# Optimization experiments

Measured on AMD Instinct MI355X. Metric: run time of the kernel, lower is better.

## Reference

```python
import jax, jax.numpy as jnp
import numpy as np

B, L, E = 512, 50, 512
VOCAB = 32000
EPS = 1e-5


def setup_inputs() -> dict:
    key = jax.random.key(0)
    ks = jax.random.split(key, 16)
    inp = {
        'src_tokens': jax.random.randint(ks[0], (B, L), 0, VOCAB, dtype=jnp.int32),
        'trg_tokens': jax.random.randint(ks[1], (B, L), 0, VOCAB, dtype=jnp.int32),
        'pad_idx': 1,
        'emb_src': jax.random.normal(ks[2], (VOCAB, E), jnp.float32) * 0.02,
        'emb_trg': jax.random.normal(ks[3], (VOCAB, E), jnp.float32) * 0.02,
        'W1': jax.random.normal(ks[4], (20, E), jnp.float32) / np.sqrt(E),  # Conv1d(1,20,k=E) kernel squeezed
        'b1': jax.random.normal(ks[5], (20,), jnp.float32) * 0.01,
        'g1': jnp.ones((20,), jnp.float32),
        'beta1': jnp.zeros((20,), jnp.float32),
        'W2': jax.random.normal(ks[6], (40, 20, 3, 3), jnp.float32) / np.sqrt(20 * 9),
        'b2': jax.random.normal(ks[7], (40,), jnp.float32) * 0.01,
        'g2': jnp.ones((40,), jnp.float32),
        'beta2': jnp.zeros((40,), jnp.float32),
        'Wfc1': jax.random.normal(ks[8], (20, 40 * 11 * 11), jnp.float32) / np.sqrt(40 * 11 * 11),
        'bfc1': jnp.zeros((20,), jnp.float32),
        'Wfc2': jax.random.normal(ks[9], (1, 20), jnp.float32) / np.sqrt(20),
        'bfc2': jnp.zeros((1,), jnp.float32),
    }
    return inp


def _maxpool2(x):  # [B,C,H,W] -> 2x2/2 valid max pool
    return jax.lax.reduce_window(x, -jnp.inf, jax.lax.max, (1, 1, 2, 2), (1, 1, 2, 2), 'VALID')


def reference(src_tokens, trg_tokens, pad_idx, emb_src, emb_trg, W1, b1, g1, beta1,
              W2, b2, g2, beta2, Wfc1, bfc1, Wfc2, bfc2):
    src_e = emb_src[src_tokens]  # [B,L,E]
    trg_e = emb_trg[trg_tokens]  # [B,L,E]

    def conv1_bn_relu(x):
        # per-sample Conv1d(1,20,k=E): collapses E -> scalar per position/channel
        f = jnp.einsum('ble,ce->blc', x, W1) + b1  # [B,L,20]
        # per-sample BatchNorm1d in training mode: stats over the L positions of each sample
        mu = jnp.mean(f, axis=1, keepdims=True)
        var = jnp.var(f, axis=1, keepdims=True)  # biased, as torch uses for normalization
        f = (f - mu) * jax.lax.rsqrt(var + EPS) * g1 + beta1
        return jax.nn.relu(f)

    s = conv1_bn_relu(src_e)  # [B,L,20]
    t = conv1_bn_relu(trg_e)  # [B,L,20]

    # broadcast outer-sum: out[b,i,j,c] = s[b,j,c] + t[b,i,c]
    out = s[:, None, :, :] + t[:, :, None, :]          # [B,L,L,20]
    out = jnp.transpose(out, (0, 3, 1, 2))             # [B,20,L,L]
    out = _maxpool2(out)                                # [B,20,25,25]

    out = jax.lax.conv_general_dilated(out, W2, (1, 1), 'VALID') + b2[None, :, None, None]  # [B,40,23,23]
    # BatchNorm2d training mode: stats over (batch, H, W)
    mu = jnp.mean(out, axis=(0, 2, 3), keepdims=True)
    var = jnp.var(out, axis=(0, 2, 3), keepdims=True)
    out = (out - mu) * jax.lax.rsqrt(var + EPS) * g2[None, :, None, None] + beta2[None, :, None, None]
    out = jax.nn.relu(out)
    out = _maxpool2(out)                                # [B,40,11,11]

    out = out.reshape(out.shape[0], -1)                 # [B,4840]
    out = out @ Wfc1.T + bfc1
    out = out @ Wfc2.T + bfc2
    return jax.nn.sigmoid(out)                          # [B,1]
```

## Files before the change

kernel.cpp:

```cpp
#include <hip/hip_runtime.h>
#include <hip/hip_bf16.h>

#define EPS 1e-5f

__device__ __forceinline__ float bf2f(unsigned short u) {
  union { unsigned int i; float f; } x; x.i = ((unsigned int)u) << 16; return x.f;
}
__device__ __forceinline__ float loadp(const void* p, int i, bool f32) {
  return f32 ? ((const float*)p)[i] : bf2f(((const unsigned short*)p)[i]);
}
__device__ __forceinline__ bool detect_f32(const void* g1) {
  return ((const unsigned int*)g1)[0] == 0x3F800000u;
}

__global__ __launch_bounds__(256) void k0_prep(
    const void* __restrict__ W1, const void* __restrict__ W2,
    const void* __restrict__ Wfc1,
    const void* __restrict__ g1, const void* __restrict__ beta1,
    const void* __restrict__ g2, const void* __restrict__ beta2,
    const void* __restrict__ bfc1, const void* __restrict__ Wfc2,
    const void* __restrict__ bfc2,
    float* __restrict__ W1T, float* __restrict__ WT, float* __restrict__ WS,
    float* __restrict__ Wfc1T, float* __restrict__ prm)
{
  const bool f32 = detect_f32(g1);
  int g = blockIdx.x * 256 + threadIdx.x;
  const int NT = 64 * 256;
  for (int i = g; i < 512 * 20; i += NT) {
    int e = i / 20, c = i - e * 20;
    W1T[i] = loadp(W1, c * 512 + e, f32);
  }
  for (int i = g; i < 40 * 3 * 20; i += NT) {
    int o = i / 60, r = i - o * 60;
    int k = r / 20, c = r - k * 20;
    float st = 0.f, ss = 0.f;
    for (int q = 0; q < 3; ++q) {
      st += loadp(W2, ((o * 20 + c) * 3 + k) * 3 + q, f32);
      ss += loadp(W2, ((o * 20 + c) * 3 + q) * 3 + k, f32);
    }
    WT[(o * 3 + k) * 20 + c] = st;
    WS[(o * 3 + k) * 20 + c] = ss;
  }
  for (int i = g; i < 4840 * 20; i += NT) {
    int kk = i / 4840, idx = i - kk * 4840;
    Wfc1T[idx * 20 + kk] = loadp(Wfc1, i, f32);
  }
  if (g < 20)        prm[g] = loadp(g1,    g,       f32);
  else if (g < 40)   prm[g] = loadp(beta1, g - 20,  f32);
  else if (g < 80)   prm[g] = loadp(g2,    g - 40,  f32);
  else if (g < 120)  prm[g] = loadp(beta2, g - 80,  f32);
  else if (g < 140)  prm[g] = loadp(bfc1,  g - 120, f32);
  else if (g < 160)  prm[g] = loadp(Wfc2,  g - 140, f32);
  else if (g == 160) prm[g] = loadp(bfc2,  0,       f32);
}

__global__ __launch_bounds__(512, 8) void k12_fused(
    const int* __restrict__ src_tok, const int* __restrict__ trg_tok,
    const void* __restrict__ emb_src, const void* __restrict__ emb_trg,
    const void* __restrict__ g1flag,
    const float* __restrict__ W1T,
    const float* __restrict__ WT, const float* __restrict__ WS,
    const float* __restrict__ prm,
    float* __restrict__ C1, float* __restrict__ R, float* __restrict__ S2)
{
  __shared__ float partA[8 * 50 * 21];
  __shared__ float fl[1000];
  __shared__ float sc[20], sh[20];
  float* wl    = partA;
  float* pmax  = partA + 2400;
  float* convl = partA + 2900;

  const bool f32 = detect_f32(g1flag);
  int bb = blockIdx.x;
  int side = bb >> 9, b = bb & 511;
  int t = threadIdx.x;
  int lane = t & 63;
  int ch = __builtin_amdgcn_readfirstlane(t >> 6);

  float acc[20];
#pragma unroll
  for (int c = 0; c < 20; ++c) acc[c] = 0.f;
  if (lane < 50) {
    int tok = side ? trg_tok[b * 50 + lane] : src_tok[b * 50 + lane];
    const void* emb = side ? emb_trg : emb_src;
    if (f32) {
      const float4* rowp = (const float4*)((const float*)emb + (size_t)tok * 512 + ch * 64);
      for (int half = 0; half < 2; ++half) {
        float4 u[8];
#pragma unroll
        for (int q = 0; q < 8; ++q) u[q] = rowp[half * 8 + q];
#pragma unroll
        for (int q = 0; q < 8; ++q) {
          float v[4] = { u[q].x, u[q].y, u[q].z, u[q].w };
          const float* w = W1T + (ch * 64 + half * 32 + q * 4) * 20;
#pragma unroll
          for (int j = 0; j < 4; ++j)
#pragma unroll
            for (int c = 0; c < 20; ++c) acc[c] = fmaf(v[j], w[j * 20 + c], acc[c]);
        }
      }
    } else {
      const uint4* rowp = (const uint4*)((const unsigned short*)emb + (size_t)tok * 512 + ch * 64);
      uint4 u[8];
#pragma unroll
      for (int q = 0; q < 8; ++q) u[q] = rowp[q];
#pragma unroll
      for (int q = 0; q < 8; ++q) {
        const unsigned int* qu = (const unsigned int*)&u[q];
        float v[8];
#pragma unroll
        for (int j = 0; j < 4; ++j) {
          union { unsigned int i; float f; } lo, hi;
          lo.i = qu[j] << 16; hi.i = qu[j] & 0xffff0000u;
          v[2 * j] = lo.f; v[2 * j + 1] = hi.f;
        }
        const float* w = W1T + (ch * 64 + q * 8) * 20;
#pragma unroll
        for (int j = 0; j < 8; ++j)
#pragma unroll
          for (int c = 0; c < 20; ++c) acc[c] = fmaf(v[j], w[j * 20 + c], acc[c]);
      }
    }
    float* pp = &partA[(ch * 50 + lane) * 21];
#pragma unroll
    for (int c = 0; c < 20; ++c) pp[c] = acc[c];
  }
  __syncthreads();
  for (int i = t; i < 1000; i += 512) {
    int l = i / 20, c = i - l * 20;
    float s = 0.f;
#pragma unroll
    for (int c2 = 0; c2 < 8; ++c2) s += partA[(c2 * 50 + l) * 21 + c];
    fl[i] = s;
  }
  __syncthreads();
  {
    const float* wsrc = side ? WT : WS;
    for (int i = t; i < 2400; i += 512) wl[i] = wsrc[i];
  }
  if (t < 20) {
    float s = 0.f, s2 = 0.f;
#pragma unroll
    for (int l = 0; l < 50; ++l) { float v = fl[l * 20 + t]; s += v; s2 += v * v; }
    float mu = s * (1.0f / 50.0f);
    float var = s2 * (1.0f / 50.0f) - mu * mu;
    float k = prm[t] * rsqrtf(var + EPS);
    sc[t] = k; sh[t] = prm[20 + t] - k * mu;
  }
  __syncthreads();
  for (int i = t; i < 500; i += 512) {
    int p = i / 20, c = i - p * 20;
    float k = sc[c], s0 = sh[c];
    float v0 = fmaxf(k * fl[(2 * p) * 20 + c] + s0, 0.f);
    float v1 = fmaxf(k * fl[(2 * p + 1) * 20 + c] + s0, 0.f);
    pmax[i] = fmaxf(v0, v1);
  }
  __syncthreads();
  for (int i = t; i < 920; i += 512) {
    int o = i / 23, y = i - o * 23;
    float a = 0.f;
#pragma unroll
    for (int ky = 0; ky < 3; ++ky) {
      const float* wr = &wl[(o * 3 + ky) * 20];
      const float* pr = &pmax[(y + ky) * 20];
#pragma unroll
      for (int c = 0; c < 20; ++c) a = fmaf(wr[c], pr[c], a);
    }
    C1[((size_t)o * 1024 + bb) * 23 + y] = a;
    convl[o * 24 + y] = a;
  }
  __syncthreads();
  if (t < 40) {
    float s = 0.f, s2 = 0.f;
#pragma unroll
    for (int y = 0; y < 23; ++y) { float v = convl[t * 24 + y]; s += v; s2 += v * v; }
    R[t * 1024 + bb] = s;
    S2[t * 1024 + bb] = s2;
  }
}

__global__ __launch_bounds__(256) void k3_bn2(
    const float* __restrict__ R, const float* __restrict__ S2,
    const float* __restrict__ prm,
    float* __restrict__ bn2)
{
  int o = blockIdx.x, t = threadIdx.x;
  float s1a = 0, s2a = 0, s1b = 0, s2b = 0, sab = 0;
  for (int b = t; b < 512; b += 256) {
    float ra = R[o * 1024 + 512 + b], rb = R[o * 1024 + b];
    s1a += ra; s1b += rb; sab += ra * rb;
    s2a += S2[o * 1024 + 512 + b];
    s2b += S2[o * 1024 + b];
  }
  __shared__ float Rd[5][256];
  Rd[0][t] = s1a; Rd[1][t] = s2a; Rd[2][t] = s1b; Rd[3][t] = s2b; Rd[4][t] = sab;
  __syncthreads();
  for (int s = 128; s > 0; s >>= 1) {
    if (t < s) {
#pragma unroll
      for (int q = 0; q < 5; ++q) Rd[q][t] += Rd[q][t + s];
    }
    __syncthreads();
  }
  if (t == 0) {
    const float invN = 1.0f / (512.0f * 23.0f);
    float muA = Rd[0][0] * invN, muB = Rd[2][0] * invN;
    float ea2 = Rd[1][0] * invN - muA * muA;
    float eb2 = Rd[3][0] * invN - muB * muB;
    float cross = 2.0f * (Rd[4][0] * (1.0f / (529.0f * 512.0f)) - muA * muB);
    float var = ea2 + eb2 + cross;
    float k = prm[40 + o] * rsqrtf(var + EPS);
    bn2[o] = k;
    bn2[40 + o] = prm[80 + o] - k * (muA + muB);
  }
}

__global__ __launch_bounds__(512) void k4_fc(
    const float* __restrict__ C1,
    const float* __restrict__ bn2,
    const float* __restrict__ Wfc1T,
    const float* __restrict__ prm,
    const void* __restrict__ g1flag,
    void* __restrict__ outv)
{
  const bool f32 = detect_f32(g1flag);
  int b = blockIdx.x, t = threadIdx.x;
  int lane = t & 63, wv = t >> 6;
  __shared__ float mA[440], mB[440];
  __shared__ float k2s[40], c2s[40];
  __shared__ float wred[8][20];
  __shared__ float o1[20];
  if (t < 40) k2s[t] = bn2[t];
  else if (t < 80) c2s[t - 40] = bn2[t];
  __syncthreads();
  for (int i = t; i < 440; i += 512) {
    int o = i / 11, y = i - o * 11;
    const float* pa = C1 + ((size_t)o * 1024 + 512 + b) * 23;
    const float* pb = C1 + ((size_t)o * 1024 + b) * 23;
    float a0 = pa[2 * y], a1 = pa[2 * y + 1];
    float b0 = pb[2 * y], b1 = pb[2 * y + 1];
    if (k2s[o] >= 0.f) { mA[i] = fmaxf(a0, a1); mB[i] = fmaxf(b0, b1); }
    else               { mA[i] = fminf(a0, a1); mB[i] = fminf(b0, b1); }
  }
  __syncthreads();
  float acc[20];
#pragma unroll
  for (int c = 0; c < 20; ++c) acc[c] = 0.f;
  for (int idx = t; idx < 4840; idx += 512) {
    int o = idx / 121, r = idx - o * 121;
    int y = r / 11, x = r - y * 11;
    float p = fmaxf(k2s[o] * (mA[o * 11 + y] + mB[o * 11 + x]) + c2s[o], 0.f);
    const float* w = Wfc1T + idx * 20;
#pragma unroll
    for (int c = 0; c < 20; ++c) acc[c] = fmaf(p, w[c], acc[c]);
  }
#pragma unroll
  for (int c = 0; c < 20; ++c) {
    float v = acc[c];
    v += __shfl_xor(v, 32); v += __shfl_xor(v, 16); v += __shfl_xor(v, 8);
    v += __shfl_xor(v, 4);  v += __shfl_xor(v, 2);  v += __shfl_xor(v, 1);
    acc[c] = v;
  }
  if (lane == 0) {
#pragma unroll
    for (int c = 0; c < 20; ++c) wred[wv][c] = acc[c];
  }
  __syncthreads();
  if (t < 20) {
    float s = 0.f;
#pragma unroll
    for (int q = 0; q < 8; ++q) s += wred[q][t];
    o1[t] = s + prm[120 + t];
  }
  __syncthreads();
  if (t == 0) {
    float z = prm[160];
#pragma unroll
    for (int c = 0; c < 20; ++c) z = fmaf(prm[140 + c], o1[c], z);
    float sg = 1.0f / (1.0f + expf(-z));
    if (f32) ((float*)outv)[b] = sg;
    else     ((__hip_bfloat16*)outv)[b] = __float2bfloat16(sg);
  }
}

extern "C" void kernel_launch(void* const* d_in, const int* in_sizes, int n_in,
                              void* d_out, int out_size, void* d_ws, size_t ws_size,
                              hipStream_t stream) {
  const int* src_tok = (const int*)d_in[0];
  const int* trg_tok = (const int*)d_in[1];
  const void* emb_src = d_in[3];
  const void* emb_trg = d_in[4];
  const void* W1    = d_in[5];
  const void* g1    = d_in[7];
  const void* beta1 = d_in[8];
  const void* W2    = d_in[9];
  const void* g2    = d_in[11];
  const void* beta2 = d_in[12];
  const void* Wfc1  = d_in[13];
  const void* bfc1  = d_in[14];
  const void* Wfc2  = d_in[15];
  const void* bfc2  = d_in[16];

  char* ws = (char*)d_ws;
  float* W1T   = (float*)(ws + 0);
  float* WT    = (float*)(ws + 40960);
  float* WS    = (float*)(ws + 50560);
  float* Wfc1T = (float*)(ws + 60160);
  float* prm   = (float*)(ws + 447360);
  float* bn2   = (float*)(ws + 448384);
  float* R     = (float*)(ws + 448896);
  float* S2    = (float*)(ws + 612736);
  float* C1    = (float*)(ws + 776576);

  k0_prep<<<64, 256, 0, stream>>>(W1, W2, Wfc1, g1, beta1, g2, beta2, bfc1, Wfc2,
                                  bfc2, W1T, WT, WS, Wfc1T, prm);
  k12_fused<<<1024, 512, 0, stream>>>(src_tok, trg_tok, emb_src, emb_trg, g1,
                                      W1T, WT, WS, prm, C1, R, S2);
  k3_bn2<<<40, 256, 0, stream>>>(R, S2, prm, bn2);
  k4_fc<<<512, 512, 0, stream>>>(C1, bn2, Wfc1T, prm, g1, d_out);
}
```

Before: 202.9 us.

## Halve k12 block size, compact LDS into one buffer, make C1/R/S2 sample-major

The fused embedding/conv kernel now runs 256 threads per block, with 4 waves each covering 128 embedding elements instead of 8 waves covering 64. Its shared arrays are merged into a single 4200-float buffer, cutting LDS per block so more blocks can be resident. C1, R and S2 are now stored sample-major, giving contiguous writes per block, and the k3/k4 readers are updated to match. Sched barriers keep the embedding loads grouped ahead of the FMAs. In exchange, each wave does more serial FMA work with fewer waves in flight per block.

```diff
diff --git a/kernel.cpp b/kernel.cpp
--- a/kernel.cpp
+++ b/kernel.cpp
@@ -54,7 +54,7 @@
   else if (g == 160) prm[g] = loadp(bfc2,  0,       f32);
 }
 
-__global__ __launch_bounds__(512, 8) void k12_fused(
+__global__ __launch_bounds__(256, 6) void k12_fused(
     const int* __restrict__ src_tok, const int* __restrict__ trg_tok,
     const void* __restrict__ emb_src, const void* __restrict__ emb_trg,
     const void* __restrict__ g1flag,
@@ -63,12 +63,7 @@
     const float* __restrict__ prm,
     float* __restrict__ C1, float* __restrict__ R, float* __restrict__ S2)
 {
-  __shared__ float partA[8 * 50 * 21];
-  __shared__ float fl[1000];
-  __shared__ float sc[20], sh[20];
-  float* wl    = partA;
-  float* pmax  = partA + 2400;
-  float* convl = partA + 2900;
+  __shared__ float lds[4200];
 
   const bool f32 = detect_f32(g1flag);
   int bb = blockIdx.x;
@@ -84,15 +79,16 @@
     int tok = side ? trg_tok[b * 50 + lane] : src_tok[b * 50 + lane];
     const void* emb = side ? emb_trg : emb_src;
     if (f32) {
-      const float4* rowp = (const float4*)((const float*)emb + (size_t)tok * 512 + ch * 64);
-      for (int half = 0; half < 2; ++half) {
+      const float4* rowp = (const float4*)((const float*)emb + (size_t)tok * 512 + ch * 128);
+      for (int grp = 0; grp < 4; ++grp) {
         float4 u[8];
 #pragma unroll
-        for (int q = 0; q < 8; ++q) u[q] = rowp[half * 8 + q];
+        for (int q = 0; q < 8; ++q) u[q] = rowp[grp * 8 + q];
+        __builtin_amdgcn_sched_barrier(0);
 #pragma unroll
         for (int q = 0; q < 8; ++q) {
           float v[4] = { u[q].x, u[q].y, u[q].z, u[q].w };
-          const float* w = W1T + (ch * 64 + half * 32 + q * 4) * 20;
+          const float* w = W1T + (ch * 128 + grp * 32 + q * 4) * 20;
 #pragma unroll
           for (int j = 0; j < 4; ++j)
 #pragma unroll
@@ -100,82 +96,85 @@
         }
       }
     } else {
-      const uint4* rowp = (const uint4*)((const unsigned short*)emb + (size_t)tok * 512 + ch * 64);
-      uint4 u[8];
-#pragma unroll
-      for (int q = 0; q < 8; ++q) u[q] = rowp[q];
-#pragma unroll
-      for (int q = 0; q < 8; ++q) {
-        const unsigned int* qu = (const unsigned int*)&u[q];
-        float v[8];
-#pragma unroll
-        for (int j = 0; j < 4; ++j) {
-          union { unsigned int i; float f; } lo, hi;
-          lo.i = qu[j] << 16; hi.i = qu[j] & 0xffff0000u;
-          v[2 * j] = lo.f; v[2 * j + 1] = hi.f;
+      const uint4* rowp = (const uint4*)((const unsigned short*)emb + (size_t)tok * 512 + ch * 128);
+      for (int half = 0; half < 2; ++half) {
+        uint4 u[8];
+#pragma unroll
+        for (int q = 0; q < 8; ++q) u[q] = rowp[half * 8 + q];
+        __builtin_amdgcn_sched_barrier(0);
+#pragma unroll
+        for (int q = 0; q < 8; ++q) {
+          const unsigned int* qu = (const unsigned int*)&u[q];
+          float v[8];
+#pragma unroll
+          for (int j = 0; j < 4; ++j) {
+            union { unsigned int i; float f; } lo, hi;
+            lo.i = qu[j] << 16; hi.i = qu[j] & 0xffff0000u;
+            v[2 * j] = lo.f; v[2 * j + 1] = hi.f;
+          }
+          const float* w = W1T + (ch * 128 + half * 64 + q * 8) * 20;
+#pragma unroll
+          for (int j = 0; j < 8; ++j)
+#pragma unroll
+            for (int c = 0; c < 20; ++c) acc[c] = fmaf(v[j], w[j * 20 + c], acc[c]);
         }
-        const float* w = W1T + (ch * 64 + q * 8) * 20;
-#pragma unroll
-        for (int j = 0; j < 8; ++j)
-#pragma unroll
-          for (int c = 0; c < 20; ++c) acc[c] = fmaf(v[j], w[j * 20 + c], acc[c]);
       }
     }
-    float* pp = &partA[(ch * 50 + lane) * 21];
+    float* pp = &lds[(ch * 50 + lane) * 21];
 #pragma unroll
     for (int c = 0; c < 20; ++c) pp[c] = acc[c];
   }
   __syncthreads();
-  for (int i = t; i < 1000; i += 512) {
+  for (int i = t; i < 1000; i += 256) {
     int l = i / 20, c = i - l * 20;
-    float s = 0.f;
-#pragma unroll
-    for (int c2 = 0; c2 < 8; ++c2) s += partA[(c2 * 50 + l) * 21 + c];
-    fl[i] = s;
+    float s = lds[l * 21 + c] + lds[(50 + l) * 21 + c]
+            + lds[(100 + l) * 21 + c] + lds[(150 + l) * 21 + c];
+    lds[l * 21 + c] = s;
   }
   __syncthreads();
   {
     const float* wsrc = side ? WT : WS;
-    for (int i = t; i < 2400; i += 512) wl[i] = wsrc[i];
+    for (int i = t; i < 2400; i += 256) lds[1050 + i] = wsrc[i];
   }
   if (t < 20) {
     float s = 0.f, s2 = 0.f;
 #pragma unroll
-    for (int l = 0; l < 50; ++l) { float v = fl[l * 20 + t]; s += v; s2 += v * v; }
+    for (int l = 0; l < 50; ++l) { float v = lds[l * 21 + t]; s += v; s2 += v * v; }
     float mu = s * (1.0f / 50.0f);
     float var = s2 * (1.0f / 50.0f) - mu * mu;
     float k = prm[t] * rsqrtf(var + EPS);
-    sc[t] = k; sh[t] = prm[20 + t] - k * mu;
-  }
-  __syncthreads();
-  for (int i = t; i < 500; i += 512) {
+    lds[3975 + t] = k;
+    lds[3995 + t] = prm[20 + t] - k * mu;
+  }
+  __syncthreads();
+  for (int i = t; i < 500; i += 256) {
     int p = i / 20, c = i - p * 20;
-    float k = sc[c], s0 = sh[c];
-    float v0 = fmaxf(k * fl[(2 * p) * 20 + c] + s0, 0.f);
-    float v1 = fmaxf(k * fl[(2 * p + 1) * 20 + c] + s0, 0.f);
-    pmax[i] = fmaxf(v0, v1);
-  }
-  __syncthreads();
-  for (int i = t; i < 920; i += 512) {
+    float k = lds[3975 + c], s0 = lds[3995 + c];
+    float v0 = fmaxf(k * lds[(2 * p) * 21 + c] + s0, 0.f);
+    float v1 = fmaxf(k * lds[(2 * p + 1) * 21 + c] + s0, 0.f);
+    lds[3450 + p * 21 + c] = fmaxf(v0, v1);
+  }
+  __syncthreads();
+  for (int i = t; i < 920; i += 256) {
     int o = i / 23, y = i - o * 23;
     float a = 0.f;
 #pragma unroll
     for (int ky = 0; ky < 3; ++ky) {
-      const float* wr = &wl[(o * 3 + ky) * 20];
-      const float* pr = &pmax[(y + ky) * 20];
+      const float* wr = &lds[1050 + (o * 3 + ky) * 20];
+      const float* pr = &lds[3450 + (y + ky) * 21];
 #pragma unroll
       for (int c = 0; c < 20; ++c) a = fmaf(wr[c], pr[c], a);
     }
-    C1[((size_t)o * 1024 + bb) * 23 + y] = a;
-    convl[o * 24 + y] = a;
+    C1[(size_t)bb * 920 + i] = a;
+    lds[i] = a;
   }
   __syncthreads();
   if (t < 40) {
     float s = 0.f, s2 = 0.f;
 #pragma unroll
-    for (int y = 0; y < 23; ++y) { float v = convl[t * 24 + y]; s += v; s2 += v * v; }
-    R[t * 1024 + bb] = s;
-    S2[t * 1024 + bb] = s2;
+    for (int y = 0; y < 23; ++y) { float v = lds[t * 23 + y]; s += v; s2 += v * v; }
+    R[bb * 40 + t] = s;
+    S2[bb * 40 + t] = s2;
   }
 }
 
@@ -187,10 +186,10 @@
   int o = blockIdx.x, t = threadIdx.x;
   float s1a = 0, s2a = 0, s1b = 0, s2b = 0, sab = 0;
   for (int b = t; b < 512; b += 256) {
-    float ra = R[o * 1024 + 512 + b], rb = R[o * 1024 + b];
+    float ra = R[(512 + b) * 40 + o], rb = R[b * 40 + o];
     s1a += ra; s1b += rb; sab += ra * rb;
-    s2a += S2[o * 1024 + 512 + b];
-    s2b += S2[o * 1024 + b];
+    s2a += S2[(512 + b) * 40 + o];
+    s2b += S2[b * 40 + o];
   }
   __shared__ float Rd[5][256];
   Rd[0][t] = s1a; Rd[1][t] = s2a; Rd[2][t] = s1b; Rd[3][t] = s2b; Rd[4][t] = sab;
@@ -235,8 +234,8 @@
   __syncthreads();
   for (int i = t; i < 440; i += 512) {
     int o = i / 11, y = i - o * 11;
-    const float* pa = C1 + ((size_t)o * 1024 + 512 + b) * 23;
-    const float* pb = C1 + ((size_t)o * 1024 + b) * 23;
+    const float* pa = C1 + (size_t)(512 + b) * 920 + o * 23;
+    const float* pb = C1 + (size_t)b * 920 + o * 23;
     float a0 = pa[2 * y], a1 = pa[2 * y + 1];
     float b0 = pb[2 * y], b1 = pb[2 * y + 1];
     if (k2s[o] >= 0.f) { mA[i] = fmaxf(a0, a1); mB[i] = fmaxf(b0, b1); }
@@ -314,7 +313,7 @@
 
   k0_prep<<<64, 256, 0, stream>>>(W1, W2, Wfc1, g1, beta1, g2, beta2, bfc1, Wfc2,
                                   bfc2, W1T, WT, WS, Wfc1T, prm);
-  k12_fused<<<1024, 512, 0, stream>>>(src_tok, trg_tok, emb_src, emb_trg, g1,
+  k12_fused<<<1024, 256, 0, stream>>>(src_tok, trg_tok, emb_src, emb_trg, g1,
                                       W1T, WT, WS, prm, C1, R, S2);
   k3_bn2<<<40, 256, 0, stream>>>(R, S2, prm, bn2);
   k4_fc<<<512, 512, 0, stream>>>(C1, bn2, Wfc1T, prm, g1, d_out);
```

New measurement: 206.7 us. No clear change (+1.9%).

## Project whole embedding tables through W1 first, then gather projected rows

Applied to the files above, without the earlier changes.

Adds a GEMM-style kernel that multiplies every vocabulary row of both embedding tables by W1 into a compact [vocab,20] table. It streams rows contiguously into LDS with direct global-to-LDS loads and an XOR swizzle. The per-sample kernel then only gathers 20 floats per token instead of 512-wide embedding rows, and runs with 256 threads and padded LDS layouts. In exchange, more rows are processed than are actually referenced: the full vocab rather than the tokens used. An extra kernel launch and an intermediate buffer are added.

```diff
diff --git a/kernel.cpp b/kernel.cpp
--- a/kernel.cpp
+++ b/kernel.cpp
@@ -2,6 +2,9 @@
 #include <hip/hip_bf16.h>
 
 #define EPS 1e-5f
+
+#define AS1 __attribute__((address_space(1)))
+#define AS3 __attribute__((address_space(3)))
 
 __device__ __forceinline__ float bf2f(unsigned short u) {
   union { unsigned int i; float f; } x; x.i = ((unsigned int)u) << 16; return x.f;
@@ -54,115 +57,155 @@
   else if (g == 160) prm[g] = loadp(bfc2,  0,       f32);
 }
 
-__global__ __launch_bounds__(512, 8) void k12_fused(
-    const int* __restrict__ src_tok, const int* __restrict__ trg_tok,
+__global__ __launch_bounds__(256, 2) void kg_gemm(
     const void* __restrict__ emb_src, const void* __restrict__ emb_trg,
     const void* __restrict__ g1flag,
     const float* __restrict__ W1T,
+    float* __restrict__ F)
+{
+  __shared__ __align__(16) float lds[16384];
+  const bool f32 = detect_f32(g1flag);
+  int p = blockIdx.x;
+  int t = threadIdx.x;
+  int lane = t & 63;
+  int w = __builtin_amdgcn_readfirstlane(t >> 6);
+  int side = (p >= 500) ? 1 : 0;
+  const char* embb = (const char*)(side ? emb_trg : emb_src);
+  int vbase = (p - side * 500) * 64;
+
+  float acc[20];
+#pragma unroll
+  for (int c = 0; c < 20; ++c) acc[c] = 0.f;
+  const int l = lane;
+  const int lx = l & 7;
+
+  if (f32) {
+    for (int h = 0; h < 2; ++h) {
+#pragma unroll
+      for (int j = 0; j < 16; ++j) {
+        int L = w * 16 + j;
+        const char* g = embb + ((size_t)(vbase + L)) * 2048 + (size_t)h * 1024
+                      + (((lane ^ (L & 7)) & 63) << 4);
+        __builtin_amdgcn_global_load_lds((const AS1 unsigned int*)g,
+            (AS3 unsigned int*)(lds + L * 256), 16, 0, 0);
+      }
+      __syncthreads();
+      {
+        const char* bp = (const char*)lds + l * 1024;
+        const float* wq = W1T + (h * 256 + w * 64) * 20;
+#pragma unroll
+        for (int kk = 0; kk < 16; ++kk) {
+          const float4 v = *(const float4*)(bp + ((w * 16 + (kk ^ lx)) << 4));
+          const float* wp = wq + kk * 80;
+          float vv[4] = { v.x, v.y, v.z, v.w };
+#pragma unroll
+          for (int e = 0; e < 4; ++e)
+#pragma unroll
+            for (int c = 0; c < 20; ++c) acc[c] = fmaf(vv[e], wp[e * 20 + c], acc[c]);
+        }
+      }
+      __syncthreads();
+    }
+  } else {
+#pragma unroll
+    for (int j = 0; j < 16; ++j) {
+      int L = w * 16 + j;
+      const char* g = embb + ((size_t)(vbase + L)) * 1024
+                    + (((lane ^ (L & 7)) & 63) << 4);
+      __builtin_amdgcn_global_load_lds((const AS1 unsigned int*)g,
+          (AS3 unsigned int*)(lds + L * 256), 16, 0, 0);
+    }
+    __syncthreads();
+    {
+      const char* bp = (const char*)lds + l * 1024;
+      const float* wq = W1T + (w * 128) * 20;
+#pragma unroll
+      for (int kk = 0; kk < 16; ++kk) {
+        const uint4 u = *(const uint4*)(bp + ((w * 16 + (kk ^ lx)) << 4));
+        const unsigned int* qu = (const unsigned int*)&u;
+        const float* wp = wq + kk * 160;
+#pragma unroll
+        for (int d = 0; d < 4; ++d) {
+          union { unsigned int i; float f; } lo, hi;
+          lo.i = qu[d] << 16; hi.i = qu[d] & 0xffff0000u;
+#pragma unroll
+          for (int c = 0; c < 20; ++c) acc[c] = fmaf(lo.f, wp[(2 * d) * 20 + c], acc[c]);
+#pragma unroll
+          for (int c = 0; c < 20; ++c) acc[c] = fmaf(hi.f, wp[(2 * d + 1) * 20 + c], acc[c]);
+        }
+      }
+    }
+    __syncthreads();
+  }
+
+  {
+    float* pp = &lds[(w * 64 + l) * 21];
+#pragma unroll
+    for (int c = 0; c < 20; ++c) pp[c] = acc[c];
+  }
+  __syncthreads();
+  for (int i = t; i < 1280; i += 256) {
+    int ll = i / 20, c = i - ll * 20;
+    float s = lds[(0 * 64 + ll) * 21 + c] + lds[(1 * 64 + ll) * 21 + c]
+            + lds[(2 * 64 + ll) * 21 + c] + lds[(3 * 64 + ll) * 21 + c];
+    F[(size_t)p * 1280 + i] = s;
+  }
+}
+
+__global__ __launch_bounds__(256) void k12_fused(
+    const int* __restrict__ src_tok, const int* __restrict__ trg_tok,
+    const float* __restrict__ F,
     const float* __restrict__ WT, const float* __restrict__ WS,
     const float* __restrict__ prm,
     float* __restrict__ C1, float* __restrict__ R, float* __restrict__ S2)
 {
-  __shared__ float partA[8 * 50 * 21];
-  __shared__ float fl[1000];
+  __shared__ float fl[50 * 21];
+  __shared__ float wl[2400];
+  __shared__ float pmax[25 * 21];
+  __shared__ float convl[40 * 24];
   __shared__ float sc[20], sh[20];
-  float* wl    = partA;
-  float* pmax  = partA + 2400;
-  float* convl = partA + 2900;
-
-  const bool f32 = detect_f32(g1flag);
+
   int bb = blockIdx.x;
   int side = bb >> 9, b = bb & 511;
   int t = threadIdx.x;
-  int lane = t & 63;
-  int ch = __builtin_amdgcn_readfirstlane(t >> 6);
-
-  float acc[20];
-#pragma unroll
-  for (int c = 0; c < 20; ++c) acc[c] = 0.f;
-  if (lane < 50) {
-    int tok = side ? trg_tok[b * 50 + lane] : src_tok[b * 50 + lane];
-    const void* emb = side ? emb_trg : emb_src;
-    if (f32) {
-      const float4* rowp = (const float4*)((const float*)emb + (size_t)tok * 512 + ch * 64);
-      for (int half = 0; half < 2; ++half) {
-        float4 u[8];
-#pragma unroll
-        for (int q = 0; q < 8; ++q) u[q] = rowp[half * 8 + q];
-#pragma unroll
-        for (int q = 0; q < 8; ++q) {
-          float v[4] = { u[q].x, u[q].y, u[q].z, u[q].w };
-          const float* w = W1T + (ch * 64 + half * 32 + q * 4) * 20;
-#pragma unroll
-          for (int j = 0; j < 4; ++j)
-#pragma unroll
-            for (int c = 0; c < 20; ++c) acc[c] = fmaf(v[j], w[j * 20 + c], acc[c]);
-        }
-      }
-    } else {
-      const uint4* rowp = (const uint4*)((const unsigned short*)emb + (size_t)tok * 512 + ch * 64);
-      uint4 u[8];
-#pragma unroll
-      for (int q = 0; q < 8; ++q) u[q] = rowp[q];
-#pragma unroll
-      for (int q = 0; q < 8; ++q) {
-        const unsigned int* qu = (const unsigned int*)&u[q];
-        float v[8];
-#pragma unroll
-        for (int j = 0; j < 4; ++j) {
-          union { unsigned int i; float f; } lo, hi;
-          lo.i = qu[j] << 16; hi.i = qu[j] & 0xffff0000u;
-          v[2 * j] = lo.f; v[2 * j + 1] = hi.f;
-        }
-        const float* w = W1T + (ch * 64 + q * 8) * 20;
-#pragma unroll
-        for (int j = 0; j < 8; ++j)
-#pragma unroll
-          for (int c = 0; c < 20; ++c) acc[c] = fmaf(v[j], w[j * 20 + c], acc[c]);
-      }
-    }
-    float* pp = &partA[(ch * 50 + lane) * 21];
-#pragma unroll
-    for (int c = 0; c < 20; ++c) pp[c] = acc[c];
-  }
-  __syncthreads();
-  for (int i = t; i < 1000; i += 512) {
+  const int* tokp = side ? trg_tok : src_tok;
+  const float* Fs = F + (size_t)side * 32000 * 20;
+
+  for (int i = t; i < 1000; i += 256) {
     int l = i / 20, c = i - l * 20;
-    float s = 0.f;
-#pragma unroll
-    for (int c2 = 0; c2 < 8; ++c2) s += partA[(c2 * 50 + l) * 21 + c];
-    fl[i] = s;
-  }
-  __syncthreads();
+    int tok = tokp[b * 50 + l];
+    fl[l * 21 + c] = Fs[(size_t)tok * 20 + c];
+  }
   {
     const float* wsrc = side ? WT : WS;
-    for (int i = t; i < 2400; i += 512) wl[i] = wsrc[i];
-  }
+    for (int i = t; i < 2400; i += 256) wl[i] = wsrc[i];
+  }
+  __syncthreads();
   if (t < 20) {
     float s = 0.f, s2 = 0.f;
 #pragma unroll
-    for (int l = 0; l < 50; ++l) { float v = fl[l * 20 + t]; s += v; s2 += v * v; }
+    for (int l = 0; l < 50; ++l) { float v = fl[l * 21 + t]; s += v; s2 += v * v; }
     float mu = s * (1.0f / 50.0f);
     float var = s2 * (1.0f / 50.0f) - mu * mu;
     float k = prm[t] * rsqrtf(var + EPS);
     sc[t] = k; sh[t] = prm[20 + t] - k * mu;
   }
   __syncthreads();
-  for (int i = t; i < 500; i += 512) {
+  for (int i = t; i < 500; i += 256) {
     int p = i / 20, c = i - p * 20;
     float k = sc[c], s0 = sh[c];
-    float v0 = fmaxf(k * fl[(2 * p) * 20 + c] + s0, 0.f);
-    float v1 = fmaxf(k * fl[(2 * p + 1) * 20 + c] + s0, 0.f);
-    pmax[i] = fmaxf(v0, v1);
-  }
-  __syncthreads();
-  for (int i = t; i < 920; i += 512) {
+    float v0 = fmaxf(k * fl[(2 * p) * 21 + c] + s0, 0.f);
+    float v1 = fmaxf(k * fl[(2 * p + 1) * 21 + c] + s0, 0.f);
+    pmax[p * 21 + c] = fmaxf(v0, v1);
+  }
+  __syncthreads();
+  for (int i = t; i < 920; i += 256) {
     int o = i / 23, y = i - o * 23;
     float a = 0.f;
 #pragma unroll
     for (int ky = 0; ky < 3; ++ky) {
       const float* wr = &wl[(o * 3 + ky) * 20];
-      const float* pr = &pmax[(y + ky) * 20];
+      const float* pr = &pmax[(y + ky) * 21];
 #pragma unroll
       for (int c = 0; c < 20; ++c) a = fmaf(wr[c], pr[c], a);
     }
@@ -311,11 +354,12 @@
   float* R     = (float*)(ws + 448896);
   float* S2    = (float*)(ws + 612736);
   float* C1    = (float*)(ws + 776576);
+  float* F     = (float*)(ws + 4544896);
 
   k0_prep<<<64, 256, 0, stream>>>(W1, W2, Wfc1, g1, beta1, g2, beta2, bfc1, Wfc2,
                                   bfc2, W1T, WT, WS, Wfc1T, prm);
-  k12_fused<<<1024, 512, 0, stream>>>(src_tok, trg_tok, emb_src, emb_trg, g1,
-                                      W1T, WT, WS, prm, C1, R, S2);
+  kg_gemm<<<1000, 256, 0, stream>>>(emb_src, emb_trg, g1, W1T, F);
+  k12_fused<<<1024, 256, 0, stream>>>(src_tok, trg_tok, F, WT, WS, prm, C1, R, S2);
   k3_bn2<<<40, 256, 0, stream>>>(R, S2, prm, bn2);
   k4_fc<<<512, 512, 0, stream>>>(C1, bn2, Wfc1T, prm, g1, d_out);
 }
```

Measured after the change: 288.4 us. 1.42x slower.
